# Optimization experiments

Hardware: AMD Instinct MI355X
Metric: run time of the kernel (lower is better)

Reference implementation:

```python
import jax, jax.numpy as jnp
import numpy as np

# Graph sampling geometry (2-layer neighbor sampling, fanouts 16 and 10)
N0 = 1_048_576   # layer-0 src nodes (full frontier, features supplied)
N1 = 65_536      # layer-0 dst nodes == layer-1 src nodes
N2 = 4_096       # layer-1 dst nodes (seeds)
DEG0, DEG1 = 16, 10
E0, E1 = N1 * DEG0, N2 * DEG1
D_IN, D_H, D_OUT = 128, 256, 47


def _init_linear(key, out_f, in_f):
    s = 1.0 / np.sqrt(in_f)
    return jax.random.uniform(key, (out_f, in_f), jnp.float32, -s, s)


def setup_inputs() -> dict:
    key = jax.random.key(0)
    ks = jax.random.split(key, 10)
    x = jax.random.normal(ks[0], (N0, D_IN), dtype=jnp.float32)
    # CSC: indptr over dst nodes (uniform degree), indices = src node ids
    indptr0 = jnp.arange(N1 + 1, dtype=jnp.int32) * DEG0
    indices0 = jax.random.randint(ks[1], (E0,), 0, N0, dtype=jnp.int32)
    indptr1 = jnp.arange(N2 + 1, dtype=jnp.int32) * DEG1
    indices1 = jax.random.randint(ks[2], (E1,), 0, N1, dtype=jnp.int32)
    return {
        "x": x,
        "indices0": indices0, "indptr0": indptr0,
        "indices1": indices1, "indptr1": indptr1,
        "Wl0": _init_linear(ks[3], D_H, D_IN), "bl0": jnp.zeros((D_H,), jnp.float32),
        "Wr0": _init_linear(ks[4], D_H, D_IN),
        "Wl1": _init_linear(ks[5], D_H, D_H), "bl1": jnp.zeros((D_H,), jnp.float32),
        "Wr1": _init_linear(ks[6], D_H, D_H),
        "Wo": _init_linear(ks[7], D_OUT, D_H), "bo": jnp.zeros((D_OUT,), jnp.float32),
    }


def expand_indptr(indptr, num_edges):
    # gb.expand_indptr: edge e -> dst j with indptr[j] <= e < indptr[j+1]
    e = jnp.arange(num_edges, dtype=indptr.dtype)
    return jnp.searchsorted(indptr, e, side="right") - 1


def sage_conv(h, src, dst, dst_size, Wl, bl, Wr):
    # PyG SAGEConv (mean aggr): lin_l(mean_{neighbors}) + lin_r(x_dst)
    msg = h[src]                                                    # [E, d]
    summed = jax.ops.segment_sum(msg, dst, num_segments=dst_size)  # [dst, d]
    cnt = jax.ops.segment_sum(jnp.ones_like(dst, dtype=h.dtype), dst,
                              num_segments=dst_size)
    mean = summed / jnp.maximum(cnt, 1.0)[:, None]
    return mean @ Wl.T + bl + h[:dst_size] @ Wr.T


def reference(x, indices0, indptr0, indices1, indptr1,
              Wl0, bl0, Wr0, Wl1, bl1, Wr1, Wo, bo):
    # layer 0
    dst0 = expand_indptr(indptr0, E0)
    h = sage_conv(x, indices0, dst0, N1, Wl0, bl0, Wr0)
    h = jax.nn.gelu(h, approximate=False)  # dropout p=0.0 -> identity
    # layer 1
    dst1 = expand_indptr(indptr1, E1)
    h = sage_conv(h, indices1, dst1, N2, Wl1, bl1, Wr1)
    h = jax.nn.gelu(h, approximate=False)
    # final projection
    return h @ Wo.T + bo
```

## Files before the change

### kernel.cpp

```cpp
#include <hip/hip_runtime.h>
#include <math.h>

#define N0 1048576
#define N1 65536
#define N2 4096
#define DEG0 16
#define DEG1 10
#define D_IN 128
#define D_H 256
#define D_OUT 47

typedef unsigned int uint32;
typedef __attribute__((ext_vector_type(8))) short bf16x8;
typedef __attribute__((ext_vector_type(4))) float f32x4;

__device__ __forceinline__ unsigned short f2b(float x) {
    uint32 u = __float_as_uint(x);
    return (unsigned short)((u + 0x7fffu + ((u >> 16) & 1u)) >> 16);
}
__device__ __forceinline__ float b2f(unsigned short h) {
    return __uint_as_float(((uint32)h) << 16);
}
__device__ __forceinline__ float gelu_exact(float x) {
    return 0.5f * x * (1.0f + erff(x * 0.70710678118654752f));
}

__global__ __launch_bounds__(256) void split_f32_kernel(
    const float4* __restrict__ src, ushort4* __restrict__ hi,
    ushort4* __restrict__ lo, int n4)
{
    int i = blockIdx.x * 256 + threadIdx.x;
    if (i >= n4) return;
    float4 v = src[i];
    ushort4 h, l;
    h.x = f2b(v.x); l.x = f2b(v.x - b2f(h.x));
    h.y = f2b(v.y); l.y = f2b(v.y - b2f(h.y));
    h.z = f2b(v.z); l.z = f2b(v.z - b2f(h.z));
    h.w = f2b(v.w); l.w = f2b(v.w - b2f(h.w));
    hi[i] = h; lo[i] = l;
}

__global__ __launch_bounds__(256) void prep_wo_kernel(
    const float4* __restrict__ Wo, const float* __restrict__ bo,
    ushort4* __restrict__ wh, ushort4* __restrict__ wl, float* __restrict__ bo_pad)
{
    int i = blockIdx.x * 256 + threadIdx.x;
    if (i < 64 * D_H / 4) {
        int row = (i * 4) >> 8;
        float4 v = make_float4(0.f, 0.f, 0.f, 0.f);
        if (row < D_OUT) v = Wo[i];
        ushort4 h, l;
        h.x = f2b(v.x); l.x = f2b(v.x - b2f(h.x));
        h.y = f2b(v.y); l.y = f2b(v.y - b2f(h.y));
        h.z = f2b(v.z); l.z = f2b(v.z - b2f(h.z));
        h.w = f2b(v.w); l.w = f2b(v.w - b2f(h.w));
        wh[i] = h; wl[i] = l;
    }
    if (blockIdx.x == 0 && threadIdx.x < 64)
        bo_pad[threadIdx.x] = (threadIdx.x < D_OUT) ? bo[threadIdx.x] : 0.f;
}

template <int DEG, int F4>
__global__ __launch_bounds__(256) void agg_split_f32(
    const float4* __restrict__ feat, const int* __restrict__ idx,
    ushort4* __restrict__ oh, ushort4* __restrict__ ol, int ndst)
{
    const int lane  = threadIdx.x % F4;
    const int local = threadIdx.x / F4;
    const int j = blockIdx.x * (256 / F4) + local;
    if (j >= ndst) return;

    const int* ip = idx + (long)j * DEG;
    int srcs[DEG];
#pragma unroll
    for (int e = 0; e < DEG; ++e) srcs[e] = ip[e];

    float4 acc = make_float4(0.f, 0.f, 0.f, 0.f);
#pragma unroll
    for (int e = 0; e < DEG; ++e) {
        float4 v = feat[(long)srcs[e] * F4 + lane];
        acc.x += v.x; acc.y += v.y; acc.z += v.z; acc.w += v.w;
    }
    const float r = 1.0f / (float)DEG;
    acc.x *= r; acc.y *= r; acc.z *= r; acc.w *= r;
    ushort4 h, l;
    h.x = f2b(acc.x); l.x = f2b(acc.x - b2f(h.x));
    h.y = f2b(acc.y); l.y = f2b(acc.y - b2f(h.y));
    h.z = f2b(acc.z); l.z = f2b(acc.z - b2f(h.z));
    h.w = f2b(acc.w); l.w = f2b(acc.w - b2f(h.w));
    oh[(long)j * F4 + lane] = h;
    ol[(long)j * F4 + lane] = l;
}

template <int DEG, int F4>
__global__ __launch_bounds__(256) void agg_split_bf16(
    const ushort4* __restrict__ fh, const ushort4* __restrict__ fl,
    const int* __restrict__ idx,
    ushort4* __restrict__ oh, ushort4* __restrict__ ol, int ndst)
{
    const int lane  = threadIdx.x % F4;
    const int local = threadIdx.x / F4;
    const int j = blockIdx.x * (256 / F4) + local;
    if (j >= ndst) return;

    const int* ip = idx + (long)j * DEG;
    int srcs[DEG];
#pragma unroll
    for (int e = 0; e < DEG; ++e) srcs[e] = ip[e];

    float4 acc = make_float4(0.f, 0.f, 0.f, 0.f);
#pragma unroll
    for (int e = 0; e < DEG; ++e) {
        long o = (long)srcs[e] * F4 + lane;
        ushort4 h = fh[o], l = fl[o];
        acc.x += b2f(h.x) + b2f(l.x);
        acc.y += b2f(h.y) + b2f(l.y);
        acc.z += b2f(h.z) + b2f(l.z);
        acc.w += b2f(h.w) + b2f(l.w);
    }
    const float r = 1.0f / (float)DEG;
    acc.x *= r; acc.y *= r; acc.z *= r; acc.w *= r;
    ushort4 h, l;
    h.x = f2b(acc.x); l.x = f2b(acc.x - b2f(h.x));
    h.y = f2b(acc.y); l.y = f2b(acc.y - b2f(h.y));
    h.z = f2b(acc.z); l.z = f2b(acc.z - b2f(h.z));
    h.w = f2b(acc.w); l.w = f2b(acc.w - b2f(h.w));
    oh[(long)j * F4 + lane] = h;
    ol[(long)j * F4 + lane] = l;
}

template <int K1, int K2, bool GELU, bool SPLIT_OUT>
__global__ __launch_bounds__(256) void gemm_mfma(
    const unsigned short* __restrict__ A1h, const unsigned short* __restrict__ A1l,
    const unsigned short* __restrict__ A2h, const unsigned short* __restrict__ A2l,
    const unsigned short* __restrict__ B1h, const unsigned short* __restrict__ B1l,
    const unsigned short* __restrict__ B2h, const unsigned short* __restrict__ B2l,
    const float* __restrict__ bias,
    float* __restrict__ Cf, unsigned short* __restrict__ Ch, unsigned short* __restrict__ Cl,
    int ldc, int ncols)
{
    constexpr int BK = 32, LDK = 40;
    __shared__ unsigned short sA[2][128][LDK];
    __shared__ unsigned short sB[2][64][LDK];

    const int tid  = threadIdx.x;
    const int bm   = blockIdx.x, bn = blockIdx.y;
    const int w    = tid >> 6;
    const int lane = tid & 63;
    const int quad = lane >> 4;
    const int l16  = lane & 15;

    f32x4 acc[2][4];
#pragma unroll
    for (int mt = 0; mt < 2; ++mt)
#pragma unroll
        for (int nt = 0; nt < 4; ++nt) acc[mt][nt] = (f32x4)0.f;

    constexpr int KT = (K1 + K2) / BK;
    for (int kt = 0; kt < KT; ++kt) {
        const int k0 = kt * BK;
        const unsigned short *Ah, *Al, *Bh, *Bl;
        int ka, koff;
        if (k0 < K1) { Ah = A1h; Al = A1l; Bh = B1h; Bl = B1l; ka = K1; koff = k0; }
        else         { Ah = A2h; Al = A2l; Bh = B2h; Bl = B2l; ka = (K2 ? K2 : 1); koff = k0 - K1; }

#pragma unroll
        for (int rep = 0; rep < 2; ++rep) {
            int task = tid + rep * 256;
            int row = task >> 2, seg = task & 3;
            size_t g = (size_t)(bm * 128 + row) * ka + koff + seg * 8;
            *(uint4*)&sA[0][row][seg * 8] = *(const uint4*)(Ah + g);
            *(uint4*)&sA[1][row][seg * 8] = *(const uint4*)(Al + g);
        }
        {
            int row = tid >> 2, seg = tid & 3;
            size_t g = (size_t)(bn * 64 + row) * ka + koff + seg * 8;
            *(uint4*)&sB[0][row][seg * 8] = *(const uint4*)(Bh + g);
            *(uint4*)&sB[1][row][seg * 8] = *(const uint4*)(Bl + g);
        }
        __syncthreads();

        bf16x8 Afh[2], Afl[2], Bfh[4], Bfl[4];
#pragma unroll
        for (int mt = 0; mt < 2; ++mt) {
            int r = w * 32 + mt * 16 + l16;
            Afh[mt] = *(const bf16x8*)&sA[0][r][quad * 8];
            Afl[mt] = *(const bf16x8*)&sA[1][r][quad * 8];
        }
#pragma unroll
        for (int nt = 0; nt < 4; ++nt) {
            int r = nt * 16 + l16;
            Bfh[nt] = *(const bf16x8*)&sB[0][r][quad * 8];
            Bfl[nt] = *(const bf16x8*)&sB[1][r][quad * 8];
        }
#pragma unroll
        for (int mt = 0; mt < 2; ++mt)
#pragma unroll
            for (int nt = 0; nt < 4; ++nt) {
                acc[mt][nt] = __builtin_amdgcn_mfma_f32_16x16x32_bf16(
                    Afl[mt], Bfh[nt], acc[mt][nt], 0, 0, 0);
                acc[mt][nt] = __builtin_amdgcn_mfma_f32_16x16x32_bf16(
                    Afh[mt], Bfl[nt], acc[mt][nt], 0, 0, 0);
                acc[mt][nt] = __builtin_amdgcn_mfma_f32_16x16x32_bf16(
                    Afh[mt], Bfh[nt], acc[mt][nt], 0, 0, 0);
            }
        __syncthreads();
    }

#pragma unroll
    for (int mt = 0; mt < 2; ++mt) {
        const int row0 = bm * 128 + w * 32 + mt * 16 + quad * 4;
#pragma unroll
        for (int nt = 0; nt < 4; ++nt) {
            const int col = bn * 64 + nt * 16 + l16;
            const float bb = bias[col];
#pragma unroll
            for (int r = 0; r < 4; ++r) {
                float v = acc[mt][nt][r] + bb;
                if (GELU) v = gelu_exact(v);
                if (SPLIT_OUT) {
                    unsigned short h = f2b(v);
                    Ch[(size_t)(row0 + r) * ldc + col] = h;
                    Cl[(size_t)(row0 + r) * ldc + col] = f2b(v - b2f(h));
                } else {
                    if (col < ncols) Cf[(size_t)(row0 + r) * ldc + col] = v;
                }
            }
        }
    }
}

extern "C" void kernel_launch(void* const* d_in, const int* in_sizes, int n_in,
                              void* d_out, int out_size, void* d_ws, size_t ws_size,
                              hipStream_t stream)
{
    const float* x        = (const float*)d_in[0];
    const int*   indices0 = (const int*)d_in[1];
    const int*   indices1 = (const int*)d_in[3];
    const float* Wl0 = (const float*)d_in[5];
    const float* bl0 = (const float*)d_in[6];
    const float* Wr0 = (const float*)d_in[7];
    const float* Wl1 = (const float*)d_in[8];
    const float* bl1 = (const float*)d_in[9];
    const float* Wr1 = (const float*)d_in[10];
    const float* Wo  = (const float*)d_in[11];
    const float* bo  = (const float*)d_in[12];
    float* out = (float*)d_out;

    unsigned short* p = (unsigned short*)d_ws;
    unsigned short* xh   = p; p += (size_t)N1 * D_IN;
    unsigned short* xl   = p; p += (size_t)N1 * D_IN;
    unsigned short* m0h  = p; p += (size_t)N1 * D_IN;
    unsigned short* m0l  = p; p += (size_t)N1 * D_IN;
    unsigned short* h0h  = p; p += (size_t)N1 * D_H;
    unsigned short* h0l  = p; p += (size_t)N1 * D_H;
    unsigned short* m1h  = p; p += (size_t)N2 * D_H;
    unsigned short* m1l  = p; p += (size_t)N2 * D_H;
    unsigned short* h1h  = p; p += (size_t)N2 * D_H;
    unsigned short* h1l  = p; p += (size_t)N2 * D_H;
    unsigned short* wl0h = p; p += 256 * 128;
    unsigned short* wl0l = p; p += 256 * 128;
    unsigned short* wr0h = p; p += 256 * 128;
    unsigned short* wr0l = p; p += 256 * 128;
    unsigned short* wl1h = p; p += 256 * 256;
    unsigned short* wl1l = p; p += 256 * 256;
    unsigned short* wr1h = p; p += 256 * 256;
    unsigned short* wr1l = p; p += 256 * 256;
    unsigned short* woh  = p; p += 64 * 256;
    unsigned short* wol  = p; p += 64 * 256;
    float* bo_pad = (float*)p;

    split_f32_kernel<<<32, 256, 0, stream>>>((const float4*)Wl0, (ushort4*)wl0h, (ushort4*)wl0l, 256 * 128 / 4);
    split_f32_kernel<<<32, 256, 0, stream>>>((const float4*)Wr0, (ushort4*)wr0h, (ushort4*)wr0l, 256 * 128 / 4);
    split_f32_kernel<<<64, 256, 0, stream>>>((const float4*)Wl1, (ushort4*)wl1h, (ushort4*)wl1l, 256 * 256 / 4);
    split_f32_kernel<<<64, 256, 0, stream>>>((const float4*)Wr1, (ushort4*)wr1h, (ushort4*)wr1l, 256 * 256 / 4);
    prep_wo_kernel<<<16, 256, 0, stream>>>((const float4*)Wo, bo, (ushort4*)woh, (ushort4*)wol, bo_pad);
    split_f32_kernel<<<(N1 * D_IN / 4 + 255) / 256, 256, 0, stream>>>(
        (const float4*)x, (ushort4*)xh, (ushort4*)xl, N1 * D_IN / 4);

    agg_split_f32<DEG0, D_IN / 4><<<N1 / (256 / (D_IN / 4)), 256, 0, stream>>>(
        (const float4*)x, indices0, (ushort4*)m0h, (ushort4*)m0l, N1);

    gemm_mfma<D_IN, D_IN, true, true><<<dim3(N1 / 128, D_H / 64), 256, 0, stream>>>(
        m0h, m0l, xh, xl, wl0h, wl0l, wr0h, wr0l, bl0,
        nullptr, h0h, h0l, D_H, D_H);

    agg_split_bf16<DEG1, D_H / 4><<<N2 / (256 / (D_H / 4)), 256, 0, stream>>>(
        (const ushort4*)h0h, (const ushort4*)h0l, indices1, (ushort4*)m1h, (ushort4*)m1l, N2);

    gemm_mfma<D_H, D_H, true, true><<<dim3(N2 / 128, D_H / 64), 256, 0, stream>>>(
        m1h, m1l, h0h, h0l, wl1h, wl1l, wr1h, wr1l, bl1,
        nullptr, h1h, h1l, D_H, D_H);

    gemm_mfma<D_H, 0, false, false><<<dim3(N2 / 128, 1), 256, 0, stream>>>(
        h1h, h1l, h1h, h1l, woh, wol, woh, wol, bo_pad,
        out, nullptr, nullptr, D_OUT, D_OUT);
}
```

Measured before the change: 809.5 us.

## Fuse layer-0 gather-mean, x split and GEMM into one kernel; merge weight prep

Layer-0 aggregation of x rows, the bf16 hi/lo split of x and the aggregated means, and the MFMA GEMM with GELU now run in one kernel per 128-row tile. The aggregated rows stay in registers and are written into shared memory per K-tile instead of being stored to and reloaded from global memory. Separate weight-split launches are merged into one prep kernel. In exchange, each block keeps 32 ushort4 registers of aggregated data, runs the four output column tiles serially with only 512 blocks, and gets no load/compute double buffering, so occupancy and overlap may suffer.

New measurement: 772.4 us (median of 2 runs). 4.6% less time.

```diff
diff --git a/kernel.cpp b/kernel.cpp
--- a/kernel.cpp
+++ b/kernel.cpp
@@ -24,72 +24,43 @@
 __device__ __forceinline__ float gelu_exact(float x) {
     return 0.5f * x * (1.0f + erff(x * 0.70710678118654752f));
 }
-
-__global__ __launch_bounds__(256) void split_f32_kernel(
-    const float4* __restrict__ src, ushort4* __restrict__ hi,
-    ushort4* __restrict__ lo, int n4)
-{
-    int i = blockIdx.x * 256 + threadIdx.x;
-    if (i >= n4) return;
-    float4 v = src[i];
-    ushort4 h, l;
+__device__ __forceinline__ void split4(const float4 v, ushort4& h, ushort4& l) {
     h.x = f2b(v.x); l.x = f2b(v.x - b2f(h.x));
     h.y = f2b(v.y); l.y = f2b(v.y - b2f(h.y));
     h.z = f2b(v.z); l.z = f2b(v.z - b2f(h.z));
     h.w = f2b(v.w); l.w = f2b(v.w - b2f(h.w));
-    hi[i] = h; lo[i] = l;
-}
-
-__global__ __launch_bounds__(256) void prep_wo_kernel(
-    const float4* __restrict__ Wo, const float* __restrict__ bo,
-    ushort4* __restrict__ wh, ushort4* __restrict__ wl, float* __restrict__ bo_pad)
+}
+
+__global__ __launch_bounds__(256) void prep_all(
+    const float4* __restrict__ Wl0, const float4* __restrict__ Wr0,
+    const float4* __restrict__ Wl1, const float4* __restrict__ Wr1,
+    const float4* __restrict__ Wo,  const float* __restrict__ bo,
+    ushort4* __restrict__ wl0h, ushort4* __restrict__ wl0l,
+    ushort4* __restrict__ wr0h, ushort4* __restrict__ wr0l,
+    ushort4* __restrict__ wl1h, ushort4* __restrict__ wl1l,
+    ushort4* __restrict__ wr1h, ushort4* __restrict__ wr1l,
+    ushort4* __restrict__ woh,  ushort4* __restrict__ wol,
+    float* __restrict__ bo_pad)
 {
     int i = blockIdx.x * 256 + threadIdx.x;
-    if (i < 64 * D_H / 4) {
-        int row = (i * 4) >> 8;
+    if (i >= 53248) return;
+    const float4* src; ushort4 *dh, *dl; int rel;
+    if (i < 8192)       { rel = i;         src = Wl0 + rel; dh = wl0h + rel; dl = wl0l + rel; }
+    else if (i < 16384) { rel = i - 8192;  src = Wr0 + rel; dh = wr0h + rel; dl = wr0l + rel; }
+    else if (i < 32768) { rel = i - 16384; src = Wl1 + rel; dh = wl1h + rel; dl = wl1l + rel; }
+    else if (i < 49152) { rel = i - 32768; src = Wr1 + rel; dh = wr1h + rel; dl = wr1l + rel; }
+    else {
+        rel = i - 49152;
         float4 v = make_float4(0.f, 0.f, 0.f, 0.f);
-        if (row < D_OUT) v = Wo[i];
-        ushort4 h, l;
-        h.x = f2b(v.x); l.x = f2b(v.x - b2f(h.x));
-        h.y = f2b(v.y); l.y = f2b(v.y - b2f(h.y));
-        h.z = f2b(v.z); l.z = f2b(v.z - b2f(h.z));
-        h.w = f2b(v.w); l.w = f2b(v.w - b2f(h.w));
-        wh[i] = h; wl[i] = l;
-    }
-    if (blockIdx.x == 0 && threadIdx.x < 64)
-        bo_pad[threadIdx.x] = (threadIdx.x < D_OUT) ? bo[threadIdx.x] : 0.f;
-}
-
-template <int DEG, int F4>
-__global__ __launch_bounds__(256) void agg_split_f32(
-    const float4* __restrict__ feat, const int* __restrict__ idx,
-    ushort4* __restrict__ oh, ushort4* __restrict__ ol, int ndst)
-{
-    const int lane  = threadIdx.x % F4;
-    const int local = threadIdx.x / F4;
-    const int j = blockIdx.x * (256 / F4) + local;
-    if (j >= ndst) return;
-
-    const int* ip = idx + (long)j * DEG;
-    int srcs[DEG];
-#pragma unroll
-    for (int e = 0; e < DEG; ++e) srcs[e] = ip[e];
-
-    float4 acc = make_float4(0.f, 0.f, 0.f, 0.f);
-#pragma unroll
-    for (int e = 0; e < DEG; ++e) {
-        float4 v = feat[(long)srcs[e] * F4 + lane];
-        acc.x += v.x; acc.y += v.y; acc.z += v.z; acc.w += v.w;
-    }
-    const float r = 1.0f / (float)DEG;
-    acc.x *= r; acc.y *= r; acc.z *= r; acc.w *= r;
-    ushort4 h, l;
-    h.x = f2b(acc.x); l.x = f2b(acc.x - b2f(h.x));
-    h.y = f2b(acc.y); l.y = f2b(acc.y - b2f(h.y));
-    h.z = f2b(acc.z); l.z = f2b(acc.z - b2f(h.z));
-    h.w = f2b(acc.w); l.w = f2b(acc.w - b2f(h.w));
-    oh[(long)j * F4 + lane] = h;
-    ol[(long)j * F4 + lane] = l;
+        if (((rel * 4) >> 8) < D_OUT) v = Wo[rel];
+        ushort4 h, l; split4(v, h, l);
+        woh[rel] = h; wol[rel] = l;
+        if (rel < 64) bo_pad[rel] = (rel < D_OUT) ? bo[rel] : 0.f;
+        return;
+    }
+    float4 v = *src;
+    ushort4 h, l; split4(v, h, l);
+    *dh = h; *dl = l;
 }
 
 template <int DEG, int F4>
@@ -120,11 +91,7 @@
     }
     const float r = 1.0f / (float)DEG;
     acc.x *= r; acc.y *= r; acc.z *= r; acc.w *= r;
-    ushort4 h, l;
-    h.x = f2b(acc.x); l.x = f2b(acc.x - b2f(h.x));
-    h.y = f2b(acc.y); l.y = f2b(acc.y - b2f(h.y));
-    h.z = f2b(acc.z); l.z = f2b(acc.z - b2f(h.z));
-    h.w = f2b(acc.w); l.w = f2b(acc.w - b2f(h.w));
+    ushort4 h, l; split4(acc, h, l);
     oh[(long)j * F4 + lane] = h;
     ol[(long)j * F4 + lane] = l;
 }
@@ -224,6 +191,140 @@
                     Cl[(size_t)(row0 + r) * ldc + col] = f2b(v - b2f(h));
                 } else {
                     if (col < ncols) Cf[(size_t)(row0 + r) * ldc + col] = v;
+                }
+            }
+        }
+    }
+}
+
+__global__ __launch_bounds__(256) void l0_fused(
+    const float4* __restrict__ x4, const int* __restrict__ idx0,
+    const unsigned short* __restrict__ B1h, const unsigned short* __restrict__ B1l,
+    const unsigned short* __restrict__ B2h, const unsigned short* __restrict__ B2l,
+    const float* __restrict__ bias,
+    unsigned short* __restrict__ Ch, unsigned short* __restrict__ Cl)
+{
+    constexpr int LDK = 40;
+    __shared__ int sIdx[128 * DEG0];
+    __shared__ unsigned short sA[2][128][LDK];
+    __shared__ unsigned short sB[2][64][LDK];
+
+    const int tid  = threadIdx.x;
+    const int bm   = blockIdx.x;
+    const int w    = tid >> 6;
+    const int l64  = tid & 63;
+    const int quad = l64 >> 4;
+    const int l16  = l64 & 15;
+    const int lane = tid & 31;
+    const int grp  = tid >> 5;
+
+    {
+        const int4* s = (const int4*)(idx0 + (size_t)bm * (128 * DEG0));
+        int4* d = (int4*)sIdx;
+        d[tid]       = s[tid];
+        d[tid + 256] = s[tid + 256];
+    }
+    __syncthreads();
+
+    ushort4 ah[16], al[16];
+#pragma unroll
+    for (int i = 0; i < 16; ++i) {
+        const int rb = (grp * 16 + i) * DEG0;
+        float4 a = make_float4(0.f, 0.f, 0.f, 0.f);
+#pragma unroll
+        for (int e = 0; e < DEG0; ++e) {
+            const float4 v = x4[(size_t)sIdx[rb + e] * (D_IN / 4) + lane];
+            a.x += v.x; a.y += v.y; a.z += v.z; a.w += v.w;
+        }
+        const float r = 1.0f / (float)DEG0;
+        a.x *= r; a.y *= r; a.z *= r; a.w *= r;
+        split4(a, ah[i], al[i]);
+    }
+
+    const int arow  = tid >> 1;
+    const int ahalf = tid & 1;
+
+    for (int bn = 0; bn < 4; ++bn) {
+        f32x4 acc[2][4];
+#pragma unroll
+        for (int mt = 0; mt < 2; ++mt)
+#pragma unroll
+            for (int nt = 0; nt < 4; ++nt) acc[mt][nt] = (f32x4)0.f;
+
+#pragma unroll
+        for (int kt = 0; kt < 8; ++kt) {
+            const int k0 = kt * 32;
+            if (kt < 4) {
+                if ((lane >> 3) == kt) {
+                    const int c = (lane & 7) * 4;
+#pragma unroll
+                    for (int i = 0; i < 16; ++i) {
+                        const int rr = grp * 16 + i;
+                        *(ushort4*)&sA[0][rr][c] = ah[i];
+                        *(ushort4*)&sA[1][rr][c] = al[i];
+                    }
+                }
+            } else {
+                const float4* sx = x4 + (size_t)(bm * 128 + arow) * (D_IN / 4)
+                                      + (kt - 4) * 8 + ahalf * 4;
+#pragma unroll
+                for (int q = 0; q < 4; ++q) {
+                    ushort4 h, l;
+                    split4(sx[q], h, l);
+                    const int c = ahalf * 16 + q * 4;
+                    *(ushort4*)&sA[0][arow][c] = h;
+                    *(ushort4*)&sA[1][arow][c] = l;
+                }
+            }
+            {
+                const int row = tid >> 2, seg = tid & 3;
+                const unsigned short *Bh, *Bl; int koff;
+                if (k0 < D_IN) { Bh = B1h; Bl = B1l; koff = k0; }
+                else           { Bh = B2h; Bl = B2l; koff = k0 - D_IN; }
+                const size_t g = (size_t)(bn * 64 + row) * D_IN + koff + seg * 8;
+                *(uint4*)&sB[0][row][seg * 8] = *(const uint4*)(Bh + g);
+                *(uint4*)&sB[1][row][seg * 8] = *(const uint4*)(Bl + g);
+            }
+            __syncthreads();
+
+            bf16x8 Afh[2], Afl[2];
+#pragma unroll
+            for (int mt = 0; mt < 2; ++mt) {
+                const int r = w * 32 + mt * 16 + l16;
+                Afh[mt] = *(const bf16x8*)&sA[0][r][quad * 8];
+                Afl[mt] = *(const bf16x8*)&sA[1][r][quad * 8];
+            }
+#pragma unroll
+            for (int nt = 0; nt < 4; ++nt) {
+                const int r = nt * 16 + l16;
+                const bf16x8 Bfh = *(const bf16x8*)&sB[0][r][quad * 8];
+                const bf16x8 Bfl = *(const bf16x8*)&sB[1][r][quad * 8];
+#pragma unroll
+                for (int mt = 0; mt < 2; ++mt) {
+                    acc[mt][nt] = __builtin_amdgcn_mfma_f32_16x16x32_bf16(
+                        Afl[mt], Bfh, acc[mt][nt], 0, 0, 0);
+                    acc[mt][nt] = __builtin_amdgcn_mfma_f32_16x16x32_bf16(
+                        Afh[mt], Bfl, acc[mt][nt], 0, 0, 0);
+                    acc[mt][nt] = __builtin_amdgcn_mfma_f32_16x16x32_bf16(
+                        Afh[mt], Bfh, acc[mt][nt], 0, 0, 0);
+                }
+            }
+            __syncthreads();
+        }
+
+#pragma unroll
+        for (int mt = 0; mt < 2; ++mt) {
+            const int row0 = bm * 128 + w * 32 + mt * 16 + quad * 4;
+#pragma unroll
+            for (int nt = 0; nt < 4; ++nt) {
+                const int col = bn * 64 + nt * 16 + l16;
+                const float bb = bias[col];
+#pragma unroll
+                for (int r = 0; r < 4; ++r) {
+                    float v = gelu_exact(acc[mt][nt][r] + bb);
+                    const unsigned short h = f2b(v);
+                    Ch[(size_t)(row0 + r) * D_H + col] = h;
+                    Cl[(size_t)(row0 + r) * D_H + col] = f2b(v - b2f(h));
                 }
             }
         }
@@ -248,10 +349,6 @@
     float* out = (float*)d_out;
 
     unsigned short* p = (unsigned short*)d_ws;
-    unsigned short* xh   = p; p += (size_t)N1 * D_IN;
-    unsigned short* xl   = p; p += (size_t)N1 * D_IN;
-    unsigned short* m0h  = p; p += (size_t)N1 * D_IN;
-    unsigned short* m0l  = p; p += (size_t)N1 * D_IN;
     unsigned short* h0h  = p; p += (size_t)N1 * D_H;
     unsigned short* h0l  = p; p += (size_t)N1 * D_H;
     unsigned short* m1h  = p; p += (size_t)N2 * D_H;
@@ -270,20 +367,15 @@
     unsigned short* wol  = p; p += 64 * 256;
     float* bo_pad = (float*)p;
 
-    split_f32_kernel<<<32, 256, 0, stream>>>((const float4*)Wl0, (ushort4*)wl0h, (ushort4*)wl0l, 256 * 128 / 4);
-    split_f32_kernel<<<32, 256, 0, stream>>>((const float4*)Wr0, (ushort4*)wr0h, (ushort4*)wr0l, 256 * 128 / 4);
-    split_f32_kernel<<<64, 256, 0, stream>>>((const float4*)Wl1, (ushort4*)wl1h, (ushort4*)wl1l, 256 * 256 / 4);
-    split_f32_kernel<<<64, 256, 0, stream>>>((const float4*)Wr1, (ushort4*)wr1h, (ushort4*)wr1l, 256 * 256 / 4);
-    prep_wo_kernel<<<16, 256, 0, stream>>>((const float4*)Wo, bo, (ushort4*)woh, (ushort4*)wol, bo_pad);
-    split_f32_kernel<<<(N1 * D_IN / 4 + 255) / 256, 256, 0, stream>>>(
-        (const float4*)x, (ushort4*)xh, (ushort4*)xl, N1 * D_IN / 4);
-
-    agg_split_f32<DEG0, D_IN / 4><<<N1 / (256 / (D_IN / 4)), 256, 0, stream>>>(
-        (const float4*)x, indices0, (ushort4*)m0h, (ushort4*)m0l, N1);
-
-    gemm_mfma<D_IN, D_IN, true, true><<<dim3(N1 / 128, D_H / 64), 256, 0, stream>>>(
-        m0h, m0l, xh, xl, wl0h, wl0l, wr0h, wr0l, bl0,
-        nullptr, h0h, h0l, D_H, D_H);
+    prep_all<<<208, 256, 0, stream>>>(
+        (const float4*)Wl0, (const float4*)Wr0, (const float4*)Wl1, (const float4*)Wr1,
+        (const float4*)Wo, bo,
+        (ushort4*)wl0h, (ushort4*)wl0l, (ushort4*)wr0h, (ushort4*)wr0l,
+        (ushort4*)wl1h, (ushort4*)wl1l, (ushort4*)wr1h, (ushort4*)wr1l,
+        (ushort4*)woh, (ushort4*)wol, bo_pad);
+
+    l0_fused<<<N1 / 128, 256, 0, stream>>>(
+        (const float4*)x, indices0, wl0h, wl0l, wr0h, wr0l, bl0, h0h, h0l);
 
     agg_split_bf16<DEG1, D_H / 4><<<N2 / (256 / (D_H / 4)), 256, 0, stream>>>(
         (const ushort4*)h0h, (const ushort4*)h0l, indices1, (ushort4*)m1h, (ushort4*)m1l, N2);
```
